# Optimization experiments

Measured on AMD Instinct MI355X. Metric: run time of the kernel, lower is better.

The kernel has to match this reference:

```python
import jax, jax.numpy as jnp
import numpy as np

HEADS, OUT_C = 8, 16
NEG_SLOPE = 0.2  # PyG GATConv default negative_slope


def setup_inputs() -> dict:
    key = jax.random.key(0)
    ks = jax.random.split(key, 6)
    N, E, IN = 100000, 1600000, 128
    x = jax.random.normal(ks[0], (N, IN), jnp.float32)
    edge_index = jax.random.randint(ks[1], (2, E), 0, N, dtype=jnp.int32)
    W = jax.random.normal(ks[2], (IN, HEADS * OUT_C), jnp.float32) / np.float32(np.sqrt(IN))
    att_src = jax.random.normal(ks[3], (HEADS, OUT_C), jnp.float32) * 0.1
    att_dst = jax.random.normal(ks[4], (HEADS, OUT_C), jnp.float32) * 0.1
    bias = jax.random.normal(ks[5], (HEADS * OUT_C,), jnp.float32) * 0.01
    return {"x": x, "edge_index": edge_index, "W": W,
            "att_src": att_src, "att_dst": att_dst, "bias": bias}


def reference(x, edge_index, W, att_src, att_dst, bias):
    N = x.shape[0]
    # Linear projection, split into heads: [N, H, C]
    xw = (x @ W).reshape(N, HEADS, OUT_C)
    # Add self-loops (PyG default add_self_loops=True)
    loops = jnp.arange(N, dtype=edge_index.dtype)
    src = jnp.concatenate([edge_index[0], loops])
    dst = jnp.concatenate([edge_index[1], loops])
    # Per-node attention terms [N, H], then per-edge logits
    a_s = jnp.einsum('nhc,hc->nh', xw, att_src)
    a_d = jnp.einsum('nhc,hc->nh', xw, att_dst)
    e = a_s[src] + a_d[dst]                       # [Etot, H]
    e = jnp.where(e > 0, e, NEG_SLOPE * e)        # LeakyReLU
    # Segment softmax over edges grouped by destination node
    emax = jax.ops.segment_max(e, dst, num_segments=N)
    p = jnp.exp(e - emax[dst])
    denom = jax.ops.segment_sum(p, dst, num_segments=N)
    alpha = p / (denom[dst] + 1e-16)              # [Etot, H]
    # Weighted scatter-aggregate of source messages
    out = jax.ops.segment_sum(xw[src] * alpha[:, :, None], dst, num_segments=N)
    out = out.reshape(N, HEADS * OUT_C) + bias    # concat heads + bias
    return jax.nn.relu(out)                       # act='relu', norm=None
```

## Files before the change

kernel.cpp:

```cpp
#include <hip/hip_runtime.h>
#include <math.h>

#define HEADS 8
#define OUTC 16
#define HC 128
#define NEG_SLOPE 0.2f

#define BM 128
#define BK 32
#define XPAD 132
#define CAP 64

typedef unsigned int uint;
typedef unsigned short ushort;

__device__ __forceinline__ ushort f2bf(float f) {
    uint u = __float_as_uint(f);
    u += 0x7FFFu + ((u >> 16) & 1u);
    return (ushort)(u >> 16);
}

__global__ __launch_bounds__(256, 4) void k_fused(
    const float* __restrict__ x, const float* __restrict__ W,
    const float* __restrict__ att_src, const float* __restrict__ att_dst,
    const int* __restrict__ ei,
    ushort* __restrict__ xwh, float* __restrict__ a_s, float* __restrict__ a_d,
    int* __restrict__ deg, int* __restrict__ csr,
    int N, int E, int GB) {
    __shared__ float xs[BK][XPAD];
    __shared__ float Ws[BK][XPAD];

    if (blockIdx.x >= GB) {
        int e = (blockIdx.x - GB) * 256 + threadIdx.x;
        if (e < E) {
            int src = ei[e];
            int dst = ei[E + e];
            int slot = atomicAdd(&deg[dst], 1);
            if (slot < CAP) csr[(size_t)dst * CAP + slot] = src;
        }
        return;
    }

    int t = threadIdx.x;
    int nb0 = blockIdx.x * BM;
    int tc = t & 15;
    int tr = t >> 4;

    float acc[8][8];
#pragma unroll
    for (int i = 0; i < 8; ++i)
#pragma unroll
        for (int j = 0; j < 8; ++j) acc[i][j] = 0.0f;

    for (int k0 = 0; k0 < HC; k0 += BK) {
        int kk4 = (t & 7) * 4;
#pragma unroll
        for (int p = 0; p < 4; ++p) {
            int nr = (t >> 3) + p * 32;
            int node = nb0 + nr;
            float4 v = make_float4(0.f, 0.f, 0.f, 0.f);
            if (node < N) v = *(const float4*)&x[(size_t)node * HC + k0 + kk4];
            xs[kk4 + 0][nr] = v.x;
            xs[kk4 + 1][nr] = v.y;
            xs[kk4 + 2][nr] = v.z;
            xs[kk4 + 3][nr] = v.w;
        }
        int kk = t >> 3;
        int c4 = (t & 7) * 4;
#pragma unroll
        for (int j = 0; j < 4; ++j) {
            *(float4*)&Ws[kk][c4 + j * 32] =
                *(const float4*)&W[(size_t)(k0 + kk) * HC + c4 + j * 32];
        }
        __syncthreads();

#pragma unroll 4
        for (int k = 0; k < BK; ++k) {
            float xa[8], wa[8];
            *(float4*)&xa[0] = *(const float4*)&xs[k][tr * 8];
            *(float4*)&xa[4] = *(const float4*)&xs[k][tr * 8 + 4];
            *(float4*)&wa[0] = *(const float4*)&Ws[k][tc * 8];
            *(float4*)&wa[4] = *(const float4*)&Ws[k][tc * 8 + 4];
#pragma unroll
            for (int i = 0; i < 8; ++i)
#pragma unroll
                for (int j = 0; j < 8; ++j)
                    acc[i][j] = fmaf(xa[i], wa[j], acc[i][j]);
        }
        __syncthreads();
    }

    float as8[8], ad8[8];
#pragma unroll
    for (int j = 0; j < 8; ++j) {
        as8[j] = att_src[tc * 8 + j];
        ad8[j] = att_dst[tc * 8 + j];
    }
    int h = tc >> 1;
#pragma unroll
    for (int i = 0; i < 8; ++i) {
        int node = nb0 + tr * 8 + i;
        float vs = 0.f, vd = 0.f;
        ushort h8[8];
#pragma unroll
        for (int j = 0; j < 8; ++j) {
            vs = fmaf(acc[i][j], as8[j], vs);
            vd = fmaf(acc[i][j], ad8[j], vd);
            h8[j] = f2bf(acc[i][j]);
        }
        vs += __shfl_xor(vs, 1);
        vd += __shfl_xor(vd, 1);
        if (node < N) {
            *(uint4*)&xwh[(size_t)node * HC + tc * 8] = *(uint4*)&h8[0];
            if ((tc & 1) == 0) {
                a_s[node * HEADS + h] = vs;
                a_d[node * HEADS + h] = vd;
            }
        }
    }
}

__global__ __launch_bounds__(256) void k_node(
    const int* __restrict__ deg, const int* __restrict__ csr,
    const float* __restrict__ a_s, const float* __restrict__ a_d,
    const uint* __restrict__ xwh, const float* __restrict__ bias,
    float* __restrict__ out, int N) {
    int n = blockIdx.x * 4 + (threadIdx.x >> 6);
    if (n >= N) return;
    int l = threadIdx.x & 63;
    int hB = l >> 3;

    float asn = a_s[n * HEADS + hB];
    float adn = a_d[n * HEADS + hB];

    float v = asn + adn;
    v = v > 0.0f ? v : NEG_SLOPE * v;
    float p = __expf(v);
    float den = p;
    uint w = xwh[n * 64 + l];
    float acc0 = p * __uint_as_float(w << 16);
    float acc1 = p * __uint_as_float(w & 0xFFFF0000u);

    int cnt = deg[n];
    if (cnt > CAP) cnt = CAP;
    const int* row = csr + (size_t)n * CAP;
#pragma unroll 4
    for (int i = 0; i < cnt; ++i) {
        int s = row[i];
        float vv = a_s[s * HEADS + hB] + adn;
        vv = vv > 0.0f ? vv : NEG_SLOPE * vv;
        float pp = __expf(vv);
        den += pp;
        uint ww = xwh[s * 64 + l];
        acc0 = fmaf(pp, __uint_as_float(ww << 16), acc0);
        acc1 = fmaf(pp, __uint_as_float(ww & 0xFFFF0000u), acc1);
    }

    float inv = 1.0f / (den + 1e-16f);
    float2 b = *(const float2*)&bias[2 * l];
    float r0 = acc0 * inv + b.x;
    float r1 = acc1 * inv + b.y;
    float2 o;
    o.x = r0 > 0.0f ? r0 : 0.0f;
    o.y = r1 > 0.0f ? r1 : 0.0f;
    *(float2*)&out[(size_t)n * HC + 2 * l] = o;
}

extern "C" void kernel_launch(void* const* d_in, const int* in_sizes, int n_in,
                              void* d_out, int out_size, void* d_ws, size_t ws_size,
                              hipStream_t stream) {
    const float* x       = (const float*)d_in[0];
    const int*   ei      = (const int*)d_in[1];
    const float* W       = (const float*)d_in[2];
    const float* att_src = (const float*)d_in[3];
    const float* att_dst = (const float*)d_in[4];
    const float* bias    = (const float*)d_in[5];
    float* out = (float*)d_out;

    int N = in_sizes[0] / HC;
    int E = in_sizes[1] / 2;

    ushort* xwh = (ushort*)d_ws;
    float* a_s  = (float*)(xwh + (size_t)N * HC);
    float* a_d  = a_s + (size_t)N * HEADS;
    int* deg    = (int*)(a_d + (size_t)N * HEADS);
    int* csr    = deg + N;

    hipMemsetAsync(deg, 0, (size_t)N * sizeof(int), stream);

    int GB = (N + BM - 1) / BM;
    int SB = (E + 255) / 256;
    k_fused<<<GB + SB, 256, 0, stream>>>(x, W, att_src, att_dst, ei,
                                         xwh, a_s, a_d, deg, csr, N, E, GB);

    k_node<<<(N + 3) / 4, 256, 0, stream>>>(deg, csr, a_s, a_d,
                                            (const uint*)xwh, bias, out, N);
}
```

Baseline: 281.4 us.

## Partition edge scatter by destination range and schedule scatter blocks first

The edge-scatter portion of the fused kernel now has each block handle a 2048-edge chunk, with 8 blocks per chunk each keeping only the edges whose destination falls in one eighth of the node range. The aim is to localize the atomics and CSR writes per block, which may improve L2/MALL locality on the deg and csr arrays. Each block also reads edges with vectorized int4 loads. Scatter blocks are moved ahead of the GEMM blocks in the grid so they are dispatched first. The cost is that every edge chunk is read 8 times.

```diff
diff --git a/kernel.cpp b/kernel.cpp
--- a/kernel.cpp
+++ b/kernel.cpp
@@ -10,6 +10,7 @@
 #define BK 32
 #define XPAD 132
 #define CAP 64
+#define CHUNK 2048
 
 typedef unsigned int uint;
 typedef unsigned short ushort;
@@ -26,23 +27,56 @@
     const int* __restrict__ ei,
     ushort* __restrict__ xwh, float* __restrict__ a_s, float* __restrict__ a_d,
     int* __restrict__ deg, int* __restrict__ csr,
-    int N, int E, int GB) {
+    int N, int E, int SBLK) {
     __shared__ float xs[BK][XPAD];
     __shared__ float Ws[BK][XPAD];
 
-    if (blockIdx.x >= GB) {
-        int e = (blockIdx.x - GB) * 256 + threadIdx.x;
-        if (e < E) {
-            int src = ei[e];
-            int dst = ei[E + e];
-            int slot = atomicAdd(&deg[dst], 1);
-            if (slot < CAP) csr[(size_t)dst * CAP + slot] = src;
+    if (blockIdx.x < SBLK) {
+        int b = blockIdx.x;
+        int chunk = b >> 3;
+        int r = b & 7;
+        int R8 = (N + 7) >> 3;
+        int lo = r * R8;
+        int hi = lo + R8; if (hi > N) hi = N;
+
+        int cbase = chunk * CHUNK;
+        int srcs[8], dsts[8];
+#pragma unroll
+        for (int g = 0; g < 2; ++g) {
+            int e = cbase + g * 1024 + 4 * (int)threadIdx.x;
+            if (e + 3 < E) {
+                int4 s4 = *(const int4*)&ei[e];
+                int4 d4 = *(const int4*)&ei[E + e];
+                srcs[4 * g + 0] = s4.x; srcs[4 * g + 1] = s4.y;
+                srcs[4 * g + 2] = s4.z; srcs[4 * g + 3] = s4.w;
+                dsts[4 * g + 0] = d4.x; dsts[4 * g + 1] = d4.y;
+                dsts[4 * g + 2] = d4.z; dsts[4 * g + 3] = d4.w;
+            } else {
+#pragma unroll
+                for (int j = 0; j < 4; ++j) {
+                    int ee = e + j;
+                    if (ee < E) {
+                        srcs[4 * g + j] = ei[ee];
+                        dsts[4 * g + j] = ei[E + ee];
+                    } else {
+                        dsts[4 * g + j] = -1;
+                    }
+                }
+            }
+        }
+#pragma unroll
+        for (int k = 0; k < 8; ++k) {
+            int d = dsts[k];
+            if (d >= lo && d < hi) {
+                int slot = atomicAdd(&deg[d], 1);
+                if (slot < CAP) csr[(size_t)d * CAP + slot] = srcs[k];
+            }
         }
         return;
     }
 
     int t = threadIdx.x;
-    int nb0 = blockIdx.x * BM;
+    int nb0 = (blockIdx.x - SBLK) * BM;
     int tc = t & 15;
     int tr = t >> 4;
 
@@ -189,9 +223,10 @@
     hipMemsetAsync(deg, 0, (size_t)N * sizeof(int), stream);
 
     int GB = (N + BM - 1) / BM;
-    int SB = (E + 255) / 256;
-    k_fused<<<GB + SB, 256, 0, stream>>>(x, W, att_src, att_dst, ei,
-                                         xwh, a_s, a_d, deg, csr, N, E, GB);
+    int SC = (E + CHUNK - 1) / CHUNK;
+    int SBLK = SC * 8;
+    k_fused<<<SBLK + GB, 256, 0, stream>>>(x, W, att_src, att_dst, ei,
+                                           xwh, a_s, a_d, deg, csr, N, E, SBLK);
 
     k_node<<<(N + 3) / 4, 256, 0, stream>>>(deg, csr, a_s, a_d,
                                             (const uint*)xwh, bias, out, N);
```

Measured after the change: 310.8 us. +10.4%, slower.

## Split each node's neighbor aggregation across four wavefronts with shared-memory reduction

Applied to the files above, without the earlier changes.

The aggregation kernel now assigns one block per destination node and has its four wavefronts take interleaved neighbors, with a shared-memory reduction at the end. The neighbor loop also issues four gathers ahead of the exp/FMA work to raise memory-level parallelism. The aim is to hide gather latency for nodes with around 16 neighbors. The cost is four times as many blocks, a __syncthreads, LDS traffic, and idle lanes when a node has few neighbors.

```diff
diff --git a/kernel.cpp b/kernel.cpp
--- a/kernel.cpp
+++ b/kernel.cpp
@@ -125,45 +125,78 @@
     const float* __restrict__ a_s, const float* __restrict__ a_d,
     const uint* __restrict__ xwh, const float* __restrict__ bias,
     float* __restrict__ out, int N) {
-    int n = blockIdx.x * 4 + (threadIdx.x >> 6);
-    if (n >= N) return;
+    __shared__ float red[3][4][64];
+
+    int n = blockIdx.x;
+    int w = threadIdx.x >> 6;
     int l = threadIdx.x & 63;
     int hB = l >> 3;
 
-    float asn = a_s[n * HEADS + hB];
     float adn = a_d[n * HEADS + hB];
 
-    float v = asn + adn;
-    v = v > 0.0f ? v : NEG_SLOPE * v;
-    float p = __expf(v);
-    float den = p;
-    uint w = xwh[n * 64 + l];
-    float acc0 = p * __uint_as_float(w << 16);
-    float acc1 = p * __uint_as_float(w & 0xFFFF0000u);
+    float den = 0.0f, acc0 = 0.0f, acc1 = 0.0f;
+    if (w == 0) {
+        float asn = a_s[n * HEADS + hB];
+        float v = asn + adn;
+        v = v > 0.0f ? v : NEG_SLOPE * v;
+        float p = __expf(v);
+        den = p;
+        uint t = xwh[n * 64 + l];
+        acc0 = p * __uint_as_float(t << 16);
+        acc1 = p * __uint_as_float(t & 0xFFFF0000u);
+    }
 
     int cnt = deg[n];
     if (cnt > CAP) cnt = CAP;
     const int* row = csr + (size_t)n * CAP;
-#pragma unroll 4
-    for (int i = 0; i < cnt; ++i) {
-        int s = row[i];
-        float vv = a_s[s * HEADS + hB] + adn;
-        vv = vv > 0.0f ? vv : NEG_SLOPE * vv;
-        float pp = __expf(vv);
-        den += pp;
-        uint ww = xwh[s * 64 + l];
-        acc0 = fmaf(pp, __uint_as_float(ww << 16), acc0);
-        acc1 = fmaf(pp, __uint_as_float(ww & 0xFFFF0000u), acc1);
-    }
-
-    float inv = 1.0f / (den + 1e-16f);
-    float2 b = *(const float2*)&bias[2 * l];
-    float r0 = acc0 * inv + b.x;
-    float r1 = acc1 * inv + b.y;
-    float2 o;
-    o.x = r0 > 0.0f ? r0 : 0.0f;
-    o.y = r1 > 0.0f ? r1 : 0.0f;
-    *(float2*)&out[(size_t)n * HC + 2 * l] = o;
+
+    for (int base = w; base < cnt; base += 16) {
+        int sv[4];
+#pragma unroll
+        for (int j = 0; j < 4; ++j) {
+            int i = base + 4 * j;
+            sv[j] = (i < cnt) ? row[i] : -1;
+        }
+        float as4[4];
+        uint w4[4];
+#pragma unroll
+        for (int j = 0; j < 4; ++j) {
+            if (sv[j] >= 0) {
+                as4[j] = a_s[sv[j] * HEADS + hB];
+                w4[j]  = xwh[(size_t)sv[j] * 64 + l];
+            }
+        }
+#pragma unroll
+        for (int j = 0; j < 4; ++j) {
+            if (sv[j] >= 0) {
+                float v = as4[j] + adn;
+                v = v > 0.0f ? v : NEG_SLOPE * v;
+                float p = __expf(v);
+                den += p;
+                acc0 = fmaf(p, __uint_as_float(w4[j] << 16), acc0);
+                acc1 = fmaf(p, __uint_as_float(w4[j] & 0xFFFF0000u), acc1);
+            }
+        }
+    }
+
+    red[0][w][l] = den;
+    red[1][w][l] = acc0;
+    red[2][w][l] = acc1;
+    __syncthreads();
+
+    if (w == 0) {
+        float d = red[0][0][l] + red[0][1][l] + red[0][2][l] + red[0][3][l];
+        float A = red[1][0][l] + red[1][1][l] + red[1][2][l] + red[1][3][l];
+        float B = red[2][0][l] + red[2][1][l] + red[2][2][l] + red[2][3][l];
+        float inv = 1.0f / (d + 1e-16f);
+        float2 b = *(const float2*)&bias[2 * l];
+        float r0 = A * inv + b.x;
+        float r1 = B * inv + b.y;
+        float2 o;
+        o.x = r0 > 0.0f ? r0 : 0.0f;
+        o.y = r1 > 0.0f ? r1 : 0.0f;
+        *(float2*)&out[(size_t)n * HC + 2 * l] = o;
+    }
 }
 
 extern "C" void kernel_launch(void* const* d_in, const int* in_sizes, int n_in,
@@ -193,6 +226,6 @@
     k_fused<<<GB + SB, 256, 0, stream>>>(x, W, att_src, att_dst, ei,
                                          xwh, a_s, a_d, deg, csr, N, E, GB);
 
-    k_node<<<(N + 3) / 4, 256, 0, stream>>>(deg, csr, a_s, a_d,
-                                            (const uint*)xwh, bias, out, N);
-}
+    k_node<<<N, 256, 0, stream>>>(deg, csr, a_s, a_d,
+                                  (const uint*)xwh, bias, out, N);
+}
```

After: 322.9 us. 14.7% more time.

## Distribute edge attention exp across lanes and broadcast weights via ds_bpermute

Applied to the files above, without the earlier changes.

In the per-node aggregation, each group of 8 lanes sharing a head now computes the attention exponent for 8 different edges in parallel instead of each lane redundantly computing it for every edge. The weights are then broadcast with ds_bpermute, the 8 neighbour feature loads are batched to raise memory-level parallelism, and the denominator is reduced with shuffles at the end. The LOG2E factor is folded into a_s/a_d at projection time so exp2f can replace __expf. This adds cross-lane permute traffic and some padding work for partial batches of 8.

```diff
diff --git a/kernel.cpp b/kernel.cpp
--- a/kernel.cpp
+++ b/kernel.cpp
@@ -5,6 +5,7 @@
 #define OUTC 16
 #define HC 128
 #define NEG_SLOPE 0.2f
+#define LOG2E 1.44269504f
 
 #define BM 128
 #define BK 32
@@ -113,8 +114,8 @@
         if (node < N) {
             *(uint4*)&xwh[(size_t)node * HC + tc * 8] = *(uint4*)&h8[0];
             if ((tc & 1) == 0) {
-                a_s[node * HEADS + h] = vs;
-                a_d[node * HEADS + h] = vd;
+                a_s[node * HEADS + h] = vs * LOG2E;
+                a_d[node * HEADS + h] = vd * LOG2E;
             }
         }
     }
@@ -129,34 +130,56 @@
     if (n >= N) return;
     int l = threadIdx.x & 63;
     int hB = l >> 3;
-
-    float asn = a_s[n * HEADS + hB];
+    int j8 = l & 7;
+    int bpb = (l & 56) << 2;
+
     float adn = a_d[n * HEADS + hB];
 
-    float v = asn + adn;
+    float v = a_s[n * HEADS + hB] + adn;
     v = v > 0.0f ? v : NEG_SLOPE * v;
-    float p = __expf(v);
-    float den = p;
+    float ps = exp2f(v);
     uint w = xwh[n * 64 + l];
-    float acc0 = p * __uint_as_float(w << 16);
-    float acc1 = p * __uint_as_float(w & 0xFFFF0000u);
+    float acc0 = ps * __uint_as_float(w << 16);
+    float acc1 = ps * __uint_as_float(w & 0xFFFF0000u);
+    float denp = (j8 == 0) ? ps : 0.0f;
 
     int cnt = deg[n];
     if (cnt > CAP) cnt = CAP;
     const int* row = csr + (size_t)n * CAP;
-#pragma unroll 4
-    for (int i = 0; i < cnt; ++i) {
-        int s = row[i];
-        float vv = a_s[s * HEADS + hB] + adn;
+
+    for (int base = 0; base < cnt; base += 8) {
+        int io = base + j8;
+        int sown = (io < cnt) ? row[io] : -1;
+        int sc = sown < 0 ? 0 : sown;
+        float asv = a_s[sc * HEADS + hB];
+        int svj[8];
+        uint w8[8];
+#pragma unroll
+        for (int j = 0; j < 8; ++j)
+            svj[j] = (base + j < cnt) ? row[base + j] : 0;
+#pragma unroll
+        for (int j = 0; j < 8; ++j)
+            w8[j] = xwh[(size_t)svj[j] * 64 + l];
+
+        float vv = asv + adn;
         vv = vv > 0.0f ? vv : NEG_SLOPE * vv;
-        float pp = __expf(vv);
-        den += pp;
-        uint ww = xwh[s * 64 + l];
-        acc0 = fmaf(pp, __uint_as_float(ww << 16), acc0);
-        acc1 = fmaf(pp, __uint_as_float(ww & 0xFFFF0000u), acc1);
-    }
-
-    float inv = 1.0f / (den + 1e-16f);
+        float pv = (sown >= 0) ? exp2f(vv) : 0.0f;
+        denp += pv;
+        int pvi = __float_as_int(pv);
+
+#pragma unroll
+        for (int j = 0; j < 8; ++j) {
+            float pj = __int_as_float(__builtin_amdgcn_ds_bpermute(bpb + 4 * j, pvi));
+            acc0 = fmaf(pj, __uint_as_float(w8[j] << 16), acc0);
+            acc1 = fmaf(pj, __uint_as_float(w8[j] & 0xFFFF0000u), acc1);
+        }
+    }
+
+    denp += __shfl_xor(denp, 1);
+    denp += __shfl_xor(denp, 2);
+    denp += __shfl_xor(denp, 4);
+
+    float inv = 1.0f / (denp + 1e-16f);
     float2 b = *(const float2*)&bias[2 * l];
     float r0 = acc0 * inv + b.x;
     float r1 = acc1 * inv + b.y;
```

Result: slower. 317.7 us (+12.9%).
